# Optimization experiments

Measured on AMD Instinct MI355X. Metric: run time of the kernel, lower is better.

Reference implementation:

```python
import jax, jax.numpy as jnp
import numpy as np
import math

NH, NKV, HD = 8, 1, 128
SOFTCAP = 30.0
ROPE_BASE = 500000.0


def _rope_tables(T, hd, base):
    half = hd // 2
    inv_freq = 1.0 / (base ** (np.arange(half, dtype=np.float32) / half))
    t = np.arange(T, dtype=np.float32)
    ang = np.outer(t, inv_freq)  # [T, half]
    return jnp.asarray(np.cos(ang)), jnp.asarray(np.sin(ang))


def apply_rope(x, cos, sin):
    # x: [B, T, H, hd]; cos/sin: [T, hd//2]
    half = x.shape[-1] // 2
    x1, x2 = x[..., :half], x[..., half:]
    T = x.shape[1]
    c = cos[:T][None, :, None, :]
    s = sin[:T][None, :, None, :]
    return jnp.concatenate([x1 * c - x2 * s, x1 * s + x2 * c], axis=-1)


def setup_inputs() -> dict:
    key = jax.random.key(0)
    ks = jax.random.split(key, 5)
    B, T, D = 4, 2048, 1024
    KD = NKV * HD
    x = jax.random.normal(ks[0], (B, T, D), dtype=jnp.float32)
    Wq = jax.random.normal(ks[1], (D, D), dtype=jnp.float32) * (D ** -0.5)
    Wk = jax.random.normal(ks[2], (KD, D), dtype=jnp.float32) * (D ** -0.5)
    Wv = jax.random.normal(ks[3], (KD, D), dtype=jnp.float32) * (D ** -0.5)
    Wo = jax.random.normal(ks[4], (D, D), dtype=jnp.float32) * (D ** -0.5)
    qk_gain = jnp.full((NH,), 1.5, dtype=jnp.float32)  # qk_gain_init
    cos, sin = _rope_tables(T, HD, ROPE_BASE)
    return {"x": x, "Wq": Wq, "Wk": Wk, "Wv": Wv, "Wo": Wo,
            "qk_gain": qk_gain, "cos": cos, "sin": sin}


def reference(x, Wq, Wk, Wv, Wo, qk_gain, cos, sin):
    B, T, D = x.shape
    # projections (QuantLinear with qat disabled == plain linear, no bias)
    q = (x @ Wq.T).reshape(B, T, NH, HD)
    k = (x @ Wk.T).reshape(B, T, NKV, HD)
    v = (x @ Wv.T).reshape(B, T, NKV, HD)
    q = apply_rope(q, cos, sin)
    k = apply_rope(k, cos, sin)
    # learned per-head QK gain applied to queries
    q = q * qk_gain[None, None, :, 1 - 1][..., None] if False else q * qk_gain[None, None, :, None]
    # GQA: broadcast the single kv head across NH query heads
    scale = 1.0 / math.sqrt(HD)
    scores = jnp.einsum('bqhd,bkgd->bhqk', q, k) * scale  # g==NKV==1 broadcast
    # logit softcap before masking/softmax
    scores = SOFTCAP * jnp.tanh(scores / SOFTCAP)
    causal = jnp.tril(jnp.ones((T, T), dtype=bool))
    scores = jnp.where(causal[None, None], scores, -jnp.inf)
    attn = jax.nn.softmax(scores, axis=-1)  # [B, NH, T, T]
    out = jnp.einsum('bhqk,bkgd->bqhd', attn, v).reshape(B, T, NH * HD)
    return out @ Wo.T
```

## Files before the change

### kernel.cpp

```cpp
#include <hip/hip_runtime.h>
#include <hip/hip_bf16.h>

#define B_ 4
#define T_ 2048
#define D_ 1024
#define NH_ 8
#define HD_ 128

typedef short short8 __attribute__((ext_vector_type(8)));
typedef float floatx4 __attribute__((ext_vector_type(4)));
typedef float floatx16 __attribute__((ext_vector_type(16)));

#if __has_builtin(__builtin_amdgcn_exp2f)
#define EXP2F __builtin_amdgcn_exp2f
#else
#define EXP2F exp2f
#endif
#if __has_builtin(__builtin_amdgcn_rcpf)
#define RCPF __builtin_amdgcn_rcpf
#else
__device__ __forceinline__ float RCPF(float x) { return 1.f / x; }
#endif

#if __has_builtin(__builtin_amdgcn_global_load_lds)
#define G2L(gp, lp)                                                        \
  __builtin_amdgcn_global_load_lds(                                        \
      (const __attribute__((address_space(1))) unsigned int*)(gp),         \
      (__attribute__((address_space(3))) unsigned int*)(lp), 16, 0, 0)
#else
#define G2L(gp, lp) (*(uint4*)(lp) = *(const uint4*)(gp))
#endif

__device__ __forceinline__ unsigned short f2b(float f) {
  union { float fl; unsigned int i; } v; v.fl = f;
  unsigned int r = v.i + 0x7fffu + ((v.i >> 16) & 1u);
  return (unsigned short)(r >> 16);
}
__device__ __forceinline__ unsigned int pack_bf16(float a, float b) {
  unsigned int ua = __float_as_uint(a) + 0x8000u;
  unsigned int ub = __float_as_uint(b) + 0x8000u;
  return (ua >> 16) | (ub & 0xffff0000u);
}
__device__ __forceinline__ float blo(unsigned int u) { return __uint_as_float(u << 16); }
__device__ __forceinline__ float bhi(unsigned int u) { return __uint_as_float(u & 0xffff0000u); }

__global__ __launch_bounds__(256) void cvt_kernel(
    const float* __restrict__ x,  const float* __restrict__ wq,
    const float* __restrict__ wk, const float* __restrict__ wv,
    const float* __restrict__ wo, unsigned short* __restrict__ dst)
{
  size_t i = ((size_t)blockIdx.x * 256 + threadIdx.x) * 8;
  const float* src; size_t off;
  if      (i <  8388608u) { src = x;  off = i; }
  else if (i <  9437184u) { src = wq; off = i - 8388608u; }
  else if (i <  9568256u) { src = wk; off = i - 9437184u; }
  else if (i <  9699328u) { src = wv; off = i - 9568256u; }
  else                    { src = wo; off = i - 9699328u; }
  float4 a = *(const float4*)(src + off);
  float4 b = *(const float4*)(src + off + 4);
  uint4 o;
  o.x = pack_bf16(a.x, a.y); o.y = pack_bf16(a.z, a.w);
  o.z = pack_bf16(b.x, b.y); o.w = pack_bf16(b.z, b.w);
  *(uint4*)(dst + i) = o;
}

template <bool C_F32>
__device__ __forceinline__ void gemm_body_1024(
    const unsigned short* __restrict__ Arow0,
    const unsigned short* __restrict__ Btile,
    void* __restrict__ Cb, int ldC)
{
  __shared__ unsigned short As[128 * 32];
  __shared__ unsigned short Bs[128 * 32];
  const int tid = threadIdx.x;
  const int lane = tid & 63;
  const int w = tid >> 6;
  const int wr = w >> 1, wc = w & 1;
  const int l15 = lane & 15, quad = lane >> 4;

  const unsigned short* a_src = Arow0 + (size_t)(tid >> 2) * 1024 + (tid & 3) * 8;
  const unsigned short* b_src = Btile + (size_t)(tid >> 2) * 1024 + (tid & 3) * 8;
  unsigned short* a_dst = &As[(tid >> 2) * 32 + (tid & 3) * 8];
  unsigned short* b_dst = &Bs[(tid >> 2) * 32 + (tid & 3) * 8];

  floatx4 zero = {0.f, 0.f, 0.f, 0.f};
  floatx4 acc[4][4];
#pragma unroll
  for (int i = 0; i < 4; i++)
#pragma unroll
    for (int j = 0; j < 4; j++) acc[i][j] = zero;

  for (int k0 = 0; k0 < 1024; k0 += 32) {
    __syncthreads();
    G2L(a_src + k0,         a_dst);
    G2L(a_src + 65536 + k0, a_dst + 2048);
    G2L(b_src + k0,         b_dst);
    G2L(b_src + 65536 + k0, b_dst + 2048);
    __syncthreads();
    short8 af[4], bfr[4];
#pragma unroll
    for (int i = 0; i < 4; i++)
      af[i] = *(const short8*)&As[(wr * 64 + i * 16 + l15) * 32 + quad * 8];
#pragma unroll
    for (int j = 0; j < 4; j++)
      bfr[j] = *(const short8*)&Bs[(wc * 64 + j * 16 + l15) * 32 + quad * 8];
#pragma unroll
    for (int i = 0; i < 4; i++)
#pragma unroll
      for (int j = 0; j < 4; j++)
        acc[i][j] = __builtin_amdgcn_mfma_f32_16x16x32_bf16(af[i], bfr[j], acc[i][j], 0, 0, 0);
  }
#pragma unroll
  for (int i = 0; i < 4; i++)
#pragma unroll
    for (int j = 0; j < 4; j++)
#pragma unroll
      for (int r = 0; r < 4; r++) {
        size_t off = (size_t)(wr * 64 + i * 16 + quad * 4 + r) * ldC + wc * 64 + j * 16 + l15;
        if (C_F32) ((float*)Cb)[off] = acc[i][j][r];
        else ((unsigned short*)Cb)[off] = f2b(acc[i][j][r]);
      }
}

__global__ __launch_bounds__(256) void gemm_qkv_kernel(
    const unsigned short* __restrict__ x,
    const unsigned short* __restrict__ Wq,
    const unsigned short* __restrict__ Wk,
    const unsigned short* __restrict__ Wv,
    unsigned short* __restrict__ q,
    unsigned short* __restrict__ k,
    unsigned short* __restrict__ v)
{
  const int bx = blockIdx.x, by = blockIdx.y;
  const unsigned short* Btile;
  unsigned short* C;
  int ldC, col0;
  if (by < 8) { Btile = Wq + (size_t)by * 128 * 1024; C = q; ldC = 1024; col0 = by * 128; }
  else if (by == 8) { Btile = Wk; C = k; ldC = 128; col0 = 0; }
  else { Btile = Wv; C = v; ldC = 128; col0 = 0; }
  gemm_body_1024<false>(x + (size_t)bx * 128 * 1024, Btile,
                        C + (size_t)bx * 128 * ldC + col0, ldC);
}

__global__ __launch_bounds__(256) void gemm_out_kernel(
    const unsigned short* __restrict__ ao,
    const unsigned short* __restrict__ Wo,
    float* __restrict__ out)
{
  const int bx = blockIdx.x, by = blockIdx.y;
  gemm_body_1024<true>(ao + (size_t)bx * 128 * 1024, Wo + (size_t)by * 128 * 1024,
                       out + (size_t)bx * 128 * 1024 + by * 128, 1024);
}

__global__ __launch_bounds__(256) void prep_kernel(
    unsigned short* __restrict__ q,
    unsigned short* __restrict__ k,
    const unsigned short* __restrict__ v,
    unsigned short* __restrict__ vT,
    const float* __restrict__ cosT,
    const float* __restrict__ sinT,
    const float* __restrict__ gain)
{
  __shared__ unsigned short tile[32 * 136];
  const int tid = threadIdx.x;
  if (blockIdx.x < 256) {
    const int b = blockIdx.x >> 6, t0 = (blockIdx.x & 63) * 32;
    for (int u = tid; u < 512; u += 256) {
      int r = u >> 4, c = u & 15;
      *(uint4*)&tile[r * 136 + c * 8] =
          *(const uint4*)(v + ((size_t)(b * T_ + t0 + r)) * 128 + c * 8);
    }
    __syncthreads();
    for (int u = tid; u < 512; u += 256) {
      int d = u >> 2, c = u & 3;
      short8 val;
#pragma unroll
      for (int j = 0; j < 8; j++) val[j] = (short)tile[(c * 8 + j) * 136 + d];
      *(short8*)(vT + ((size_t)(b * 128 + d)) * T_ + t0 + c * 8) = val;
    }
    return;
  }
  int idx = (blockIdx.x - 256) * 256 + tid;
  unsigned short* ptr;
  size_t base;
  int t, j;
  float g;
  if (idx < 524288) {
    j = idx & 7;
    int h = (idx >> 3) & 7;
    int bt = idx >> 6;
    t = bt & (T_ - 1);
    base = (size_t)bt * 1024 + h * 128 + j * 8;
    ptr = q;
    g = gain[h] * 0.0029462782549439484f;
  } else {
    int id = idx - 524288;
    j = id & 7;
    int bt = id >> 3;
    t = bt & (T_ - 1);
    base = (size_t)bt * 128 + j * 8;
    ptr = k;
    g = 1.f;
  }
  float4 ca = *(const float4*)&cosT[t * 64 + j * 8];
  float4 cb = *(const float4*)&cosT[t * 64 + j * 8 + 4];
  float4 sa = *(const float4*)&sinT[t * 64 + j * 8];
  float4 sb = *(const float4*)&sinT[t * 64 + j * 8 + 4];
  uint4 lo = *(const uint4*)(ptr + base);
  uint4 hi = *(const uint4*)(ptr + base + 64);
  uint4 olo, ohi;
  {
    float a0 = blo(lo.x), a1 = bhi(lo.x), b0 = blo(hi.x), b1 = bhi(hi.x);
    olo.x = pack_bf16((a0 * ca.x - b0 * sa.x) * g, (a1 * ca.y - b1 * sa.y) * g);
    ohi.x = pack_bf16((a0 * sa.x + b0 * ca.x) * g, (a1 * sa.y + b1 * ca.y) * g);
  }
  {
    float a0 = blo(lo.y), a1 = bhi(lo.y), b0 = blo(hi.y), b1 = bhi(hi.y);
    olo.y = pack_bf16((a0 * ca.z - b0 * sa.z) * g, (a1 * ca.w - b1 * sa.w) * g);
    ohi.y = pack_bf16((a0 * sa.z + b0 * ca.z) * g, (a1 * sa.w + b1 * ca.w) * g);
  }
  {
    float a0 = blo(lo.z), a1 = bhi(lo.z), b0 = blo(hi.z), b1 = bhi(hi.z);
    olo.z = pack_bf16((a0 * cb.x - b0 * sb.x) * g, (a1 * cb.y - b1 * sb.y) * g);
    ohi.z = pack_bf16((a0 * sb.x + b0 * cb.x) * g, (a1 * sb.y + b1 * cb.y) * g);
  }
  {
    float a0 = blo(lo.w), a1 = bhi(lo.w), b0 = blo(hi.w), b1 = bhi(hi.w);
    olo.w = pack_bf16((a0 * cb.z - b0 * sb.z) * g, (a1 * cb.w - b1 * sb.w) * g);
    ohi.w = pack_bf16((a0 * sb.z + b0 * cb.z) * g, (a1 * sb.w + b1 * cb.w) * g);
  }
  *(uint4*)(ptr + base) = olo;
  *(uint4*)(ptr + base + 64) = ohi;
}

template <int NSPLIT>
__global__ __launch_bounds__(256, 3) void attn_kernel(
    const unsigned short* __restrict__ q,
    const unsigned short* __restrict__ k,
    const unsigned short* __restrict__ vT,
    unsigned short* __restrict__ ao,
    unsigned short* __restrict__ Opart,
    float* __restrict__ lbuf)
{
  __shared__ unsigned short Ks[2][16 * 264];
  __shared__ unsigned short Vts[2][128 * 40];

  const int h = blockIdx.y, b = blockIdx.z;
  const int pr   = blockIdx.x / NSPLIT;
  const int part = blockIdx.x % NSPLIT;
  const int tid = threadIdx.x, lane = tid & 63, w = tid >> 6;
  const int q32 = lane & 31, hi = lane >> 5;

  const unsigned short* ksrc =
      k + (size_t)b * T_ * 128 + (size_t)(tid >> 4) * 128 + (tid & 15) * 8;
  const int koff0 = (tid & 15) * 264 + (tid >> 4) * 8;
  const int koff1 = koff0 + 16 * 8;
  const unsigned short* vsrc =
      vT + (size_t)b * 128 * T_ + (size_t)(tid >> 2) * T_ + (tid & 3) * 8;
  const int voff0 = (tid >> 2) * 40 + (tid & 3) * 8;
  const int voff1 = voff0 + 64 * 40;

  for (int pass = 0; pass < 2; pass++) {
    const int qblock = pass ? (15 - pr) : pr;
    const int qw = qblock * 128 + w * 32;
    const int nkt = 4 * qblock + 4;
    const int base = nkt / NSPLIT, rem = nkt % NSPLIT;
    const int ktBeg = part * base + (part < rem ? part : rem);
    const int ktEnd = ktBeg + base + (part < rem ? 1 : 0);

    short8 qf[8];
    {
      const unsigned short* qrow =
          q + ((size_t)(b * T_ + qw + q32) * NH_ + h) * HD_ + hi * 8;
#pragma unroll
      for (int c = 0; c < 8; c++) qf[c] = *(const short8*)(qrow + c * 16);
    }

    float l_i = 0.f;
    floatx16 acc[4];
#pragma unroll
    for (int dt = 0; dt < 4; dt++)
#pragma unroll
      for (int r = 0; r < 16; r++) acc[dt][r] = 0.f;

    __syncthreads();
    {
      uint4 kr0 = *(const uint4*)(ksrc + (size_t)ktBeg * 4096);
      uint4 kr1 = *(const uint4*)(ksrc + (size_t)ktBeg * 4096 + 2048);
      uint4 vr0 = *(const uint4*)(vsrc + ktBeg * 32);
      uint4 vr1 = *(const uint4*)(vsrc + (size_t)64 * T_ + ktBeg * 32);
      unsigned short* kb = Ks[ktBeg & 1];
      unsigned short* vb = Vts[ktBeg & 1];
      *(uint4*)(kb + koff0) = kr0; *(uint4*)(kb + koff1) = kr1;
      *(uint4*)(vb + voff0) = vr0; *(uint4*)(vb + voff1) = vr1;
    }

    for (int kt = ktBeg; kt < ktEnd; kt++) {
      __syncthreads();
      uint4 kr0, kr1, vr0, vr1;
      const bool more = (kt + 1 < ktEnd);
      if (more) {
        kr0 = *(const uint4*)(ksrc + (size_t)(kt + 1) * 4096);
        kr1 = *(const uint4*)(ksrc + (size_t)(kt + 1) * 4096 + 2048);
        vr0 = *(const uint4*)(vsrc + (kt + 1) * 32);
        vr1 = *(const uint4*)(vsrc + (size_t)64 * T_ + (kt + 1) * 32);
      }

      if (kt * 32 <= qw + 31) {
        const unsigned short* KsC = Ks[kt & 1];
        const unsigned short* VtC = Vts[kt & 1];
        floatx16 st;
#pragma unroll
        for (int r = 0; r < 16; r++) st[r] = 0.f;
#pragma unroll
        for (int c = 0; c < 8; c++) {
          short8 kf = *(const short8*)&KsC[(2 * c + hi) * 264 + q32 * 8];
          st = __builtin_amdgcn_mfma_f32_32x32x16_bf16(kf, qf[c], st, 0, 0, 0);
        }
        float rs = 0.f;
        unsigned int A[8];
        if (kt * 32 + 31 <= qw) {
          float pv[16];
#pragma unroll
          for (int r = 0; r < 16; r++) {
            float s = st[r];
            float e = EXP2F(2.8853901f * s);
            float u = RCPF(e + 1.f);
            float p = EXP2F(-86.561707f * u);
            pv[r] = p;
            rs += p;
          }
#pragma unroll
          for (int m = 0; m < 8; m++) A[m] = pack_bf16(pv[2 * m], pv[2 * m + 1]);
        } else {
          const int qrow = qw + q32;
          float pv[16];
#pragma unroll
          for (int r = 0; r < 16; r++) {
            float s = st[r];
            float e = EXP2F(2.8853901f * s);
            float u = RCPF(e + 1.f);
            float p = EXP2F(-86.561707f * u);
            int key = kt * 32 + (r & 3) + 8 * (r >> 2) + 4 * hi;
            p = (key <= qrow) ? p : 0.f;
            pv[r] = p;
            rs += p;
          }
#pragma unroll
          for (int m = 0; m < 8; m++) A[m] = pack_bf16(pv[2 * m], pv[2 * m + 1]);
        }
        unsigned int a0 = A[0], a1 = A[1], a2 = A[2], a3 = A[3];
        unsigned int a4 = A[4], a5 = A[5], a6 = A[6], a7 = A[7];
        asm("v_permlane32_swap_b32 %0, %1" : "+v"(a0), "+v"(a2));
        asm("v_permlane32_swap_b32 %0, %1" : "+v"(a1), "+v"(a3));
        asm("v_permlane32_swap_b32 %0, %1" : "+v"(a4), "+v"(a6));
        asm("v_permlane32_swap_b32 %0, %1" : "+v"(a5), "+v"(a7));
        uint4 u0; u0.x = a0; u0.y = a1; u0.z = a2; u0.w = a3;
        uint4 u1; u1.x = a4; u1.y = a5; u1.z = a6; u1.w = a7;
        short8 pf0 = *(short8*)&u0;
        short8 pf1 = *(short8*)&u1;
        l_i += rs + __shfl_xor(rs, 32);
#pragma unroll
        for (int dt = 0; dt < 4; dt++) {
          short8 v0 = *(const short8*)&VtC[(dt * 32 + q32) * 40 + hi * 8];
          short8 v1 = *(const short8*)&VtC[(dt * 32 + q32) * 40 + 16 + hi * 8];
          acc[dt] = __builtin_amdgcn_mfma_f32_32x32x16_bf16(v0, pf0, acc[dt], 0, 0, 0);
          acc[dt] = __builtin_amdgcn_mfma_f32_32x32x16_bf16(v1, pf1, acc[dt], 0, 0, 0);
        }
      }

      if (more) {
        unsigned short* kb = Ks[(kt + 1) & 1];
        unsigned short* vb = Vts[(kt + 1) & 1];
        *(uint4*)(kb + koff0) = kr0; *(uint4*)(kb + koff1) = kr1;
        *(uint4*)(vb + voff0) = vr0; *(uint4*)(vb + voff1) = vr1;
      }
    }

    {
      const size_t rowidx = (size_t)(b * T_ + qw + q32) * NH_ + h;
      if (NSPLIT == 1) {
        float linv = 1.f / l_i;
        unsigned short* aop = ao + rowidx * HD_;
#pragma unroll
        for (int dt = 0; dt < 4; dt++)
#pragma unroll
          for (int rg = 0; rg < 4; rg++) {
            uint2 o;
            o.x = pack_bf16(acc[dt][4 * rg + 0] * linv, acc[dt][4 * rg + 1] * linv);
            o.y = pack_bf16(acc[dt][4 * rg + 2] * linv, acc[dt][4 * rg + 3] * linv);
            *(uint2*)(aop + dt * 32 + rg * 8 + hi * 4) = o;
          }
      } else {
        unsigned short* dst =
            ((part == NSPLIT - 1) ? ao : Opart + (size_t)part * 8388608u) +
            rowidx * HD_;
#pragma unroll
        for (int dt = 0; dt < 4; dt++)
#pragma unroll
          for (int rg = 0; rg < 4; rg++) {
            uint2 o;
            o.x = pack_bf16(acc[dt][4 * rg + 0], acc[dt][4 * rg + 1]);
            o.y = pack_bf16(acc[dt][4 * rg + 2], acc[dt][4 * rg + 3]);
            *(uint2*)(dst + dt * 32 + rg * 8 + hi * 4) = o;
          }
        if (hi == 0) lbuf[(size_t)part * 65536u + rowidx] = l_i;
      }
    }
  }
}

template <int NSPLIT>
__global__ __launch_bounds__(256) void combine_kernel(
    const unsigned short* __restrict__ Opart,
    const float* __restrict__ lbuf,
    unsigned short* __restrict__ ao)
{
  size_t i = ((size_t)blockIdx.x * 256 + threadIdx.x) * 8;
  size_t r = i >> 7;
  float ls = 0.f;
#pragma unroll
  for (int p = 0; p < NSPLIT; p++) ls += lbuf[(size_t)p * 65536u + r];
  float linv = RCPF(ls);
  uint4 c = *(const uint4*)(ao + i);
  float v0 = blo(c.x), v1 = bhi(c.x), v2 = blo(c.y), v3 = bhi(c.y);
  float v4 = blo(c.z), v5 = bhi(c.z), v6 = blo(c.w), v7 = bhi(c.w);
#pragma unroll
  for (int p = 0; p < NSPLIT - 1; p++) {
    uint4 a = *(const uint4*)(Opart + (size_t)p * 8388608u + i);
    v0 += blo(a.x); v1 += bhi(a.x); v2 += blo(a.y); v3 += bhi(a.y);
    v4 += blo(a.z); v5 += bhi(a.z); v6 += blo(a.w); v7 += bhi(a.w);
  }
  uint4 o;
  o.x = pack_bf16(v0 * linv, v1 * linv);
  o.y = pack_bf16(v2 * linv, v3 * linv);
  o.z = pack_bf16(v4 * linv, v5 * linv);
  o.w = pack_bf16(v6 * linv, v7 * linv);
  *(uint4*)(ao + i) = o;
}

extern "C" void kernel_launch(void* const* d_in, const int* in_sizes, int n_in,
                              void* d_out, int out_size, void* d_ws, size_t ws_size,
                              hipStream_t stream) {
  const float* x    = (const float*)d_in[0];
  const float* Wq   = (const float*)d_in[1];
  const float* Wk   = (const float*)d_in[2];
  const float* Wv   = (const float*)d_in[3];
  const float* Wo   = (const float*)d_in[4];
  const float* gain = (const float*)d_in[5];
  const float* cosT = (const float*)d_in[6];
  const float* sinT = (const float*)d_in[7];
  float* out = (float*)d_out;

  unsigned short* ws = (unsigned short*)d_ws;
  unsigned short* blob = ws;
  unsigned short* xb  = blob;
  unsigned short* Wqb = blob + 8388608u;
  unsigned short* Wkb = blob + 9437184u;
  unsigned short* Wvb = blob + 9568256u;
  unsigned short* Wob = blob + 9699328u;
  unsigned short* q   = ws + 10747904u;
  unsigned short* kk  = ws + 19136512u;
  unsigned short* v   = ws + 20185088u;
  unsigned short* vT  = ws + 21233664u;
  unsigned short* ao  = xb;
  unsigned short* Opart = ws + 22282240u;
  float* l2 = (float*)((char*)d_ws + 61341696u);
  const size_t need2 = 61865984ull;

  cvt_kernel<<<5248, 256, 0, stream>>>(x, Wq, Wk, Wv, Wo, blob);
  gemm_qkv_kernel<<<dim3(64, 10), 256, 0, stream>>>(xb, Wqb, Wkb, Wvb, q, kk, v);
  prep_kernel<<<2560, 256, 0, stream>>>(q, kk, v, vT, cosT, sinT, gain);
  if (ws_size >= need2) {
    attn_kernel<2><<<dim3(16, 8, 4), 256, 0, stream>>>(q, kk, vT, ao, Opart, l2);
    combine_kernel<2><<<4096, 256, 0, stream>>>(Opart, l2, ao);
  } else {
    attn_kernel<1><<<dim3(8, 8, 4), 256, 0, stream>>>(q, kk, vT, ao, Opart, l2);
  }
  gemm_out_kernel<<<dim3(64, 8), 256, 0, stream>>>(ao, Wob, out);
}
```

Baseline: 232.3 us.

## Process two K/V tiles per barrier with four-slot LDS buffering

The attention inner loop now handles two 32-key tiles per iteration. It prefetches the next two tiles into a four-slot shared-memory ring, which halves the number of __syncthreads barriers and puts more global loads in flight at once. LDS use doubles, so the launch bound drops from 3 to 2 blocks per SM. The split-range computation also drops the remainder handling and assumes nkt is divisible by NSPLIT and that each segment has an even tile count. The extra prefetch registers raise register pressure.

After: 269.0 us. 15.8% more time.

```diff
diff --git a/kernel.cpp b/kernel.cpp
--- a/kernel.cpp
+++ b/kernel.cpp
@@ -234,7 +234,7 @@
 }
 
 template <int NSPLIT>
-__global__ __launch_bounds__(256, 3) void attn_kernel(
+__global__ __launch_bounds__(256, 2) void attn_kernel(
     const unsigned short* __restrict__ q,
     const unsigned short* __restrict__ k,
     const unsigned short* __restrict__ vT,
@@ -242,8 +242,8 @@
     unsigned short* __restrict__ Opart,
     float* __restrict__ lbuf)
 {
-  __shared__ unsigned short Ks[2][16 * 264];
-  __shared__ unsigned short Vts[2][128 * 40];
+  __shared__ unsigned short Ks[4][16 * 264];
+  __shared__ unsigned short Vts[4][128 * 40];
 
   const int h = blockIdx.y, b = blockIdx.z;
   const int pr   = blockIdx.x / NSPLIT;
@@ -264,9 +264,9 @@
     const int qblock = pass ? (15 - pr) : pr;
     const int qw = qblock * 128 + w * 32;
     const int nkt = 4 * qblock + 4;
-    const int base = nkt / NSPLIT, rem = nkt % NSPLIT;
-    const int ktBeg = part * base + (part < rem ? part : rem);
-    const int ktEnd = ktBeg + base + (part < rem ? 1 : 0);
+    const int seg = nkt / NSPLIT;
+    const int ktBeg = part * seg;
+    const int ktEnd = ktBeg + seg;
 
     short8 qf[8];
     {
@@ -284,31 +284,41 @@
       for (int r = 0; r < 16; r++) acc[dt][r] = 0.f;
 
     __syncthreads();
-    {
-      uint4 kr0 = *(const uint4*)(ksrc + (size_t)ktBeg * 4096);
-      uint4 kr1 = *(const uint4*)(ksrc + (size_t)ktBeg * 4096 + 2048);
-      uint4 vr0 = *(const uint4*)(vsrc + ktBeg * 32);
-      uint4 vr1 = *(const uint4*)(vsrc + (size_t)64 * T_ + ktBeg * 32);
-      unsigned short* kb = Ks[ktBeg & 1];
-      unsigned short* vb = Vts[ktBeg & 1];
+#pragma unroll
+    for (int s = 0; s < 2; s++) {
+      const int kn = ktBeg + s;
+      uint4 kr0 = *(const uint4*)(ksrc + (size_t)kn * 4096);
+      uint4 kr1 = *(const uint4*)(ksrc + (size_t)kn * 4096 + 2048);
+      uint4 vr0 = *(const uint4*)(vsrc + kn * 32);
+      uint4 vr1 = *(const uint4*)(vsrc + (size_t)64 * T_ + kn * 32);
+      unsigned short* kb = Ks[s];
+      unsigned short* vb = Vts[s];
       *(uint4*)(kb + koff0) = kr0; *(uint4*)(kb + koff1) = kr1;
       *(uint4*)(vb + voff0) = vr0; *(uint4*)(vb + voff1) = vr1;
     }
 
-    for (int kt = ktBeg; kt < ktEnd; kt++) {
+    int bp = 0;
+    for (int kt = ktBeg; kt < ktEnd; kt += 2) {
       __syncthreads();
-      uint4 kr0, kr1, vr0, vr1;
-      const bool more = (kt + 1 < ktEnd);
+      uint4 kr0[2], kr1[2], vr0[2], vr1[2];
+      const bool more = (kt + 2 < ktEnd);
       if (more) {
-        kr0 = *(const uint4*)(ksrc + (size_t)(kt + 1) * 4096);
-        kr1 = *(const uint4*)(ksrc + (size_t)(kt + 1) * 4096 + 2048);
-        vr0 = *(const uint4*)(vsrc + (kt + 1) * 32);
-        vr1 = *(const uint4*)(vsrc + (size_t)64 * T_ + (kt + 1) * 32);
+#pragma unroll
+        for (int s = 0; s < 2; s++) {
+          const int kn = kt + 2 + s;
+          kr0[s] = *(const uint4*)(ksrc + (size_t)kn * 4096);
+          kr1[s] = *(const uint4*)(ksrc + (size_t)kn * 4096 + 2048);
+          vr0[s] = *(const uint4*)(vsrc + kn * 32);
+          vr1[s] = *(const uint4*)(vsrc + (size_t)64 * T_ + kn * 32);
+        }
       }
 
-      if (kt * 32 <= qw + 31) {
-        const unsigned short* KsC = Ks[kt & 1];
-        const unsigned short* VtC = Vts[kt & 1];
+#pragma unroll
+      for (int s = 0; s < 2; s++) {
+        const int ktc = kt + s;
+        if (ktc * 32 > qw + 31) continue;
+        const unsigned short* KsC = Ks[bp + s];
+        const unsigned short* VtC = Vts[bp + s];
         floatx16 st;
 #pragma unroll
         for (int r = 0; r < 16; r++) st[r] = 0.f;
@@ -319,12 +329,12 @@
         }
         float rs = 0.f;
         unsigned int A[8];
-        if (kt * 32 + 31 <= qw) {
+        if (ktc * 32 + 31 <= qw) {
           float pv[16];
 #pragma unroll
           for (int r = 0; r < 16; r++) {
-            float s = st[r];
-            float e = EXP2F(2.8853901f * s);
+            float s2 = st[r];
+            float e = EXP2F(2.8853901f * s2);
             float u = RCPF(e + 1.f);
             float p = EXP2F(-86.561707f * u);
             pv[r] = p;
@@ -337,11 +347,11 @@
           float pv[16];
 #pragma unroll
           for (int r = 0; r < 16; r++) {
-            float s = st[r];
-            float e = EXP2F(2.8853901f * s);
+            float s2 = st[r];
+            float e = EXP2F(2.8853901f * s2);
             float u = RCPF(e + 1.f);
             float p = EXP2F(-86.561707f * u);
-            int key = kt * 32 + (r & 3) + 8 * (r >> 2) + 4 * hi;
+            int key = ktc * 32 + (r & 3) + 8 * (r >> 2) + 4 * hi;
             p = (key <= qrow) ? p : 0.f;
             pv[r] = p;
             rs += p;
@@ -370,11 +380,15 @@
       }
 
       if (more) {
-        unsigned short* kb = Ks[(kt + 1) & 1];
-        unsigned short* vb = Vts[(kt + 1) & 1];
-        *(uint4*)(kb + koff0) = kr0; *(uint4*)(kb + koff1) = kr1;
-        *(uint4*)(vb + voff0) = vr0; *(uint4*)(vb + voff1) = vr1;
+#pragma unroll
+        for (int s = 0; s < 2; s++) {
+          unsigned short* kb = Ks[(bp ^ 2) + s];
+          unsigned short* vb = Vts[(bp ^ 2) + s];
+          *(uint4*)(kb + koff0) = kr0[s]; *(uint4*)(kb + koff1) = kr1[s];
+          *(uint4*)(vb + voff0) = vr0[s]; *(uint4*)(vb + voff1) = vr1[s];
+        }
       }
+      bp ^= 2;
     }
 
     {
```
